# Kernel optimization log

Hardware: AMD Instinct MI355X
Metric: run time of the kernel (lower is better)

## Reference

```python
import jax, jax.numpy as jnp
import numpy as np

H = 5  # hidden size
SEQ = 512
BATCH = 16384


def _lstm_layer(x, Wih, Whh, bih, bhh):
    # x: (B, S, D_in); weights follow PyTorch layout: W (4H, D), gate order i,f,g,o
    B = x.shape[0]
    b = bih + bhh
    xs = jnp.swapaxes(x, 0, 1)  # (S, B, D_in)
    # precompute input projections for all timesteps: (S, B, 4H)
    xproj = jnp.einsum('sbd,gd->sbg', xs, Wih) + b

    def step(carry, xp):
        h, c = carry
        gates = xp + h @ Whh.T  # (B, 4H)
        i, f, g, o = jnp.split(gates, 4, axis=-1)
        i = jax.nn.sigmoid(i)
        f = jax.nn.sigmoid(f)
        g = jnp.tanh(g)
        o = jax.nn.sigmoid(o)
        c = f * c + i * g
        h = o * jnp.tanh(c)
        return (h, c), h

    h0 = jnp.zeros((B, H), dtype=x.dtype)
    c0 = jnp.zeros((B, H), dtype=x.dtype)
    _, hs = jax.lax.scan(step, (h0, c0), xproj)  # hs: (S, B, H)
    return jnp.swapaxes(hs, 0, 1)  # (B, S, H)


def setup_inputs() -> dict:
    key = jax.random.key(0)
    ks = jax.random.split(key, 13)
    s = 1.0 / np.sqrt(H)
    u = lambda k, shp: jax.random.uniform(k, shp, jnp.float32, -s, s)
    return {
        'x': jax.random.normal(ks[0], (BATCH, SEQ, 1), jnp.float32),
        'Wih0': u(ks[1], (4 * H, 1)),
        'Whh0': u(ks[2], (4 * H, H)),
        'bih0': u(ks[3], (4 * H,)),
        'bhh0': u(ks[4], (4 * H,)),
        'Wih1': u(ks[5], (4 * H, H)),
        'Whh1': u(ks[6], (4 * H, H)),
        'bih1': u(ks[7], (4 * H,)),
        'bhh1': u(ks[8], (4 * H,)),
        'W1': jax.random.uniform(ks[9], (512, SEQ * H), jnp.float32, -1 / np.sqrt(SEQ * H), 1 / np.sqrt(SEQ * H)),
        'b1': jax.random.uniform(ks[10], (512,), jnp.float32, -1 / np.sqrt(SEQ * H), 1 / np.sqrt(SEQ * H)),
        'W2': jax.random.uniform(ks[11], (1, 512), jnp.float32, -1 / np.sqrt(512), 1 / np.sqrt(512)),
        'b2': jax.random.uniform(ks[12], (1,), jnp.float32, -1 / np.sqrt(512), 1 / np.sqrt(512)),
    }


def reference(x, Wih0, Whh0, bih0, bhh0, Wih1, Whh1, bih1, bhh1, W1, b1, W2, b2):
    h = _lstm_layer(x, Wih0, Whh0, bih0, bhh0)   # (B, S, 5)
    h = _lstm_layer(h, Wih1, Whh1, bih1, bhh1)   # (B, S, 5)
    h = h.reshape(h.shape[0], -1)                # (B, S*5)
    h = h @ W1.T + b1                            # (B, 512)
    out = h @ W2.T + b2                          # (B, 1)
    return out
```

## Files before the change

kernel.cpp:

```cpp
#include <hip/hip_runtime.h>

#define BATCH 16384
#define SEQ 512

typedef float f4 __attribute__((ext_vector_type(4)));
typedef _Float16 half4 __attribute__((ext_vector_type(4)));
typedef _Float16 half8 __attribute__((ext_vector_type(8)));

#define SIGS (-1.44269504088896f)
#define TNHS (-2.88539008177793f)
#define NTNH (2.88539008177793f)

union HB2 { unsigned int u[2]; half4 h; };
union HB4 { unsigned int u[4]; half8 h; };

__device__ __forceinline__ float bpermf(int addr, float v) {
    return __int_as_float(__builtin_amdgcn_ds_bpermute(addr, __float_as_int(v)));
}
__device__ __forceinline__ unsigned int h16(float v) {
    return (unsigned int)__builtin_bit_cast(unsigned short, (_Float16)v);
}
__device__ __forceinline__ unsigned int pk2(float a, float b) {
    return __builtin_bit_cast(unsigned int, __builtin_amdgcn_cvt_pkrtz(a, b));
}
__device__ __forceinline__ unsigned int lolo(unsigned int a, unsigned int b) {
    return __builtin_amdgcn_perm(b, a, 0x05040100u);
}

__global__ __launch_bounds__(256) void collapse_kernel(
    const float* __restrict__ W1, const float* __restrict__ b1,
    const float* __restrict__ W2, const float* __restrict__ b2,
    float* __restrict__ ws)
{
    const int kl = threadIdx.x & 15;
    const int ms = threadIdx.x >> 4;
    const int k  = blockIdx.x * 16 + kl;
    const float* w1p = W1 + (size_t)(ms * 32) * 2560 + k;
    const float* w2p = W2 + ms * 32;
    float acc = 0.f;
    #pragma unroll 8
    for (int m = 0; m < 32; ++m) acc = fmaf(w2p[m], w1p[(size_t)m * 2560], acc);
    __shared__ float red[16][17];
    red[ms][kl] = acc;
    __syncthreads();
    if (ms == 0) {
        float s = 0.f;
        #pragma unroll
        for (int r = 0; r < 16; ++r) s += red[r][kl];
        const int t = k / 5, u = k % 5;
        if (u < 4) ws[(u << 10) + 2 * t] = s;
        else {
            ws[2*t + 1] = s;        ws[1024 + 2*t + 1] = s;
            ws[2048 + 2*t + 1] = s; ws[3072 + 2*t + 1] = s;
        }
    }
    if (blockIdx.x == 0) {
        const int t = threadIdx.x;
        float p = fmaf(W2[t], b1[t], W2[t + 256] * b1[t + 256]);
        #pragma unroll
        for (int off = 32; off > 0; off >>= 1) p += __shfl_down(p, off);
        __shared__ float cred[4];
        if ((t & 63) == 0) cred[t >> 6] = p;
        __syncthreads();
        if (t == 0) ws[4096] = cred[0] + cred[1] + cred[2] + cred[3] + b2[0];
    }
}

__global__ __launch_bounds__(64)
__attribute__((amdgpu_waves_per_eu(1, 1)))
void lstm_fused_kernel(
    const float* __restrict__ x,
    const float* __restrict__ Wih0, const float* __restrict__ Whh0,
    const float* __restrict__ bih0, const float* __restrict__ bhh0,
    const float* __restrict__ Wih1, const float* __restrict__ Whh1,
    const float* __restrict__ bih1, const float* __restrict__ bhh1,
    const float* __restrict__ ws, float* __restrict__ out)
{
    const int lane = threadIdx.x;
    const int e15  = lane & 15;
    const int g    = lane >> 4;
    const int e    = blockIdx.x * 16 + e15;
    const float sc[4] = {SIGS, SIGS, TNHS, SIGS};

    HB2 aL0a, aL1a;
    HB4 aU;
    {
        const int m = e15;
        {
            const int u = m >> 2, gi = m & 3, gr = gi * 5 + u;
            const float s = sc[gi];
            float w0 = Whh0[gr * 5 + g];
            float w1 = (g == 0) ? Wih0[gr] : (g == 1 ? Whh0[gr * 5 + 4] : 0.f);
            aL0a.u[0] = h16(w0 * s) | (h16(w1 * s) << 16);
            aL0a.u[1] = 0u;
        }
        {
            const int u = m >> 2, gi = m & 3, gr = gi * 5 + u;
            const float s = sc[gi];
            float w0 = Wih1[gr * 5 + g];
            float w1 = Whh1[gr * 5 + g];
            float w2 = (g == 1) ? Wih1[gr * 5 + 4] : (g == 2 ? Whh1[gr * 5 + 4] : 0.f);
            aL1a.u[0] = h16(w0 * s) | (h16(w1 * s) << 16);
            aL1a.u[1] = h16(w2 * s);
        }
        {
            float w0 = 0.f, w1 = 0.f, s = 0.f;
            if (m >= 4 && m < 8) {
                const int gi = m - 4, gr = gi * 5 + 4;
                s = sc[gi];
                w0 = Whh0[gr * 5 + g];
                w1 = (g == 0) ? Wih0[gr] : (g == 1 ? Whh0[gr * 5 + 4] : 0.f);
            }
            aU.u[0] = h16(w0 * s) | (h16(w1 * s) << 16);
            aU.u[1] = 0u;
        }
        {
            float w0 = 0.f, w1 = 0.f, w2 = 0.f, s = 0.f;
            if (m >= 8 && m < 12) {
                const int gi = m - 8, gr = gi * 5 + 4;
                s = sc[gi];
                w0 = Wih1[gr * 5 + g];
                w1 = Whh1[gr * 5 + g];
                w2 = (g == 1) ? Wih1[gr * 5 + 4] : (g == 2 ? Whh1[gr * 5 + 4] : 0.f);
            }
            aU.u[2] = h16(w0 * s) | (h16(w1 * s) << 16);
            aU.u[3] = h16(w2 * s);
        }
    }
    f4 cL0a, cL1a, cbm;
    #pragma unroll
    for (int r = 0; r < 4; ++r) {
        cL0a[r] = (bih0[r*5+g] + bhh0[r*5+g]) * sc[r];
        cL1a[r] = (bih1[r*5+g] + bhh1[r*5+g]) * sc[r];
        cbm[r]  = (g == 1) ? (bih0[r*5+4] + bhh0[r*5+4]) * sc[r]
                : (g == 2) ? (bih1[r*5+4] + bhh1[r*5+4]) * sc[r] : 0.f;
    }

    const float* xp  = x + (size_t)e * SEQ;
    const float* wsg = ws + (g << 10);
    const bool isg0 = (g == 0), isg2 = (g == 2);
    const unsigned selA = isg0 ? 0x05040100u : 0x03020100u;
    const unsigned selB = isg0 ? 0x07060100u : 0x03020100u;

    float cs0 = 0.f, cs1 = 0.f, cs4 = 0.f, acc = 0.f, acc4 = 0.f;
    f4 dA, dC, dU;

    {
        float2 x01 = *(const float2*)xp;
        unsigned xh0 = h16(x01.x), xh1 = h16(x01.y);
        HB2 b0; b0.u[0] = isg0 ? (xh0 << 16) : 0u; b0.u[1] = 0u;
        dA = __builtin_amdgcn_mfma_f32_16x16x16f16(aL0a.h, b0.h, cL0a, 0, 0, 0);
        HB4 bu0; bu0.u[0] = b0.u[0]; bu0.u[1] = bu0.u[2] = bu0.u[3] = 0u;
        dU = __builtin_amdgcn_mfma_f32_16x16x32_f16(aU.h, bu0.h, cbm, 0, 0, 0);
        float A0 = __builtin_amdgcn_exp2f(dA[0]), F0 = __builtin_amdgcn_exp2f(dA[1]);
        float B0 = __builtin_amdgcn_exp2f(dA[2]), O0 = __builtin_amdgcn_exp2f(dA[3]);
        float A1 = __builtin_amdgcn_exp2f(dU[0]), F1 = __builtin_amdgcn_exp2f(dU[1]);
        float B1 = __builtin_amdgcn_exp2f(dU[2]), O1 = __builtin_amdgcn_exp2f(dU[3]);
        float t0 = 1.f + A0, t1 = 1.f + A1;
        float ab0 = fmaf(t0, B0, t0), ab1 = fmaf(t1, B1, t1);
        float D0 = fmaf(ab0, F0, ab0), D1 = fmaf(ab1, F1, ab1);
        float r0 = __builtin_amdgcn_rcpf(D0), r1 = __builtin_amdgcn_rcpf(D1);
        float bs0 = fmaf(B0, NTNH, TNHS), bs1 = fmaf(B1, NTNH, TNHS);
        float w0 = fmaf(bs0, F0, bs0), w1 = fmaf(bs1, F1, bs1);
        cs0 = fmaf(ab0, cs0, w0) * r0;
        cs4 = fmaf(ab1, cs4, w1) * r1;
        float Ce0 = __builtin_amdgcn_exp2f(fminf(cs0, 17.f));
        float Ce1 = __builtin_amdgcn_exp2f(fminf(cs4, 17.f));
        float o0 = 1.f + O0, o1 = 1.f + O1;
        float e0 = fmaf(o0, Ce0, o0), e1 = fmaf(o1, Ce1, o1);
        float hA = (1.f - Ce0) * __builtin_amdgcn_rcpf(e0);
        float h4 = (1.f - Ce1) * __builtin_amdgcn_rcpf(e1);
        if (isg2) { h4 = 0.f; cs4 = 0.f; }
        unsigned hx0 = pk2(hA, h4);
        HB2 B0n, B1n;
        B0n.u[0] = isg0 ? lolo(hx0, xh1) : hx0;  B0n.u[1] = 0u;
        dA = __builtin_amdgcn_mfma_f32_16x16x16f16(aL0a.h, B0n.h, cL0a, 0, 0, 0);
        B1n.u[0] = pk2(hA, 0.f);  B1n.u[1] = hx0 >> 16;
        HB4 BU; BU.u[0] = B0n.u[0]; BU.u[1] = 0u; BU.u[2] = B1n.u[0]; BU.u[3] = B1n.u[1];
        dU = __builtin_amdgcn_mfma_f32_16x16x32_f16(aU.h, BU.h, cbm, 0, 0, 0);
        dC = __builtin_amdgcn_mfma_f32_16x16x16f16(aL1a.h, B1n.h, cL1a, 0, 0, 0);
    }

    auto body = [&](unsigned xpair, unsigned sel, float wMu, float w4u) {
        float A0 = __builtin_amdgcn_exp2f(dA[0]), F0 = __builtin_amdgcn_exp2f(dA[1]);
        float B0 = __builtin_amdgcn_exp2f(dA[2]), O0 = __builtin_amdgcn_exp2f(dA[3]);
        float A1 = __builtin_amdgcn_exp2f(dU[0]), F1 = __builtin_amdgcn_exp2f(dU[1]);
        float B1 = __builtin_amdgcn_exp2f(dU[2]), O1 = __builtin_amdgcn_exp2f(dU[3]);
        float A2 = __builtin_amdgcn_exp2f(dC[0]), F2 = __builtin_amdgcn_exp2f(dC[1]);
        float B2 = __builtin_amdgcn_exp2f(dC[2]), O2 = __builtin_amdgcn_exp2f(dC[3]);
        float t0 = 1.f + A0, t1 = 1.f + A1, t2 = 1.f + A2;
        float ab0 = fmaf(t0, B0, t0), ab1 = fmaf(t1, B1, t1), ab2 = fmaf(t2, B2, t2);
        float D0 = fmaf(ab0, F0, ab0), D1 = fmaf(ab1, F1, ab1), D2 = fmaf(ab2, F2, ab2);
        float r01 = __builtin_amdgcn_rcpf(D0 * D1);
        float r0 = r01 * D1, r1 = r01 * D0;
        float r2 = __builtin_amdgcn_rcpf(D2);
        float bs0 = fmaf(B0, NTNH, TNHS), bs1 = fmaf(B1, NTNH, TNHS), bs2 = fmaf(B2, NTNH, TNHS);
        float w0 = fmaf(bs0, F0, bs0), w1 = fmaf(bs1, F1, bs1), w2 = fmaf(bs2, F2, bs2);
        cs0 = fmaf(ab0, cs0, w0) * r0;
        cs4 = fmaf(ab1, cs4, w1) * r1;
        cs1 = fmaf(ab2, cs1, w2) * r2;
        float Ce2 = __builtin_amdgcn_exp2f(fminf(cs1, 17.f));
        float o2 = 1.f + O2;
        float e2 = fmaf(o2, Ce2, o2);
        float hC = (1.f - Ce2) * __builtin_amdgcn_rcpf(e2);
        acc  = fmaf(hC, wMu, acc);
        float Ce0 = __builtin_amdgcn_exp2f(fminf(cs0, 17.f));
        float Ce1 = __builtin_amdgcn_exp2f(fminf(cs4, 17.f));
        float o0 = 1.f + O0, o1 = 1.f + O1;
        float e0 = fmaf(o0, Ce0, o0), e1 = fmaf(o1, Ce1, o1);
        float rr = __builtin_amdgcn_rcpf(e0 * e1);
        float hA = (1.f - Ce0) * (rr * e1);
        float h4 = (1.f - Ce1) * (rr * e0);
        acc4 = fmaf(h4, w4u, acc4);
        unsigned hx0  = pk2(hA, h4);
        unsigned b1lo = pk2(hA, hC);
        unsigned b1hi = hx0 >> 16;
        HB2 B0n;
        B0n.u[0] = __builtin_amdgcn_perm(xpair, hx0, sel);  B0n.u[1] = 0u;
        dA = __builtin_amdgcn_mfma_f32_16x16x16f16(aL0a.h, B0n.h, cL0a, 0, 0, 0);
        HB4 BU; BU.u[0] = B0n.u[0]; BU.u[1] = 0u; BU.u[2] = b1lo; BU.u[3] = b1hi;
        dU = __builtin_amdgcn_mfma_f32_16x16x32_f16(aU.h, BU.h, cbm, 0, 0, 0);
        HB2 B1n; B1n.u[0] = b1lo; B1n.u[1] = b1hi;
        dC = __builtin_amdgcn_mfma_f32_16x16x16f16(aL1a.h, B1n.h, cL1a, 0, 0, 0);
    };

    unsigned xqa, xqb;  float4 wqa, wqb;
    {
        float2 xi0 = *(const float2*)(xp + 2);
        float2 xi1 = *(const float2*)(xp + 4);
        xqa = pk2(xi0.x, xi0.y);  xqb = pk2(xi1.x, xi1.y);
        wqa = *(const float4*)(wsg);
        wqb = *(const float4*)(wsg + 4);
    }
    for (int m = 1; m < 502; m += 4) {
        float2 xi0 = *(const float2*)(xp + m + 5);
        float2 xi1 = *(const float2*)(xp + m + 7);
        unsigned nxa = pk2(xi0.x, xi0.y), nxb = pk2(xi1.x, xi1.y);
        float4 nwa = *(const float4*)(wsg + 2 * (m + 3));
        float4 nwb = *(const float4*)(wsg + 2 * (m + 3) + 4);
        body(xqa, selA, wqa.x, wqa.y);
        body(xqa, selB, wqa.z, wqa.w);
        body(xqb, selA, wqb.x, wqb.y);
        body(xqb, selB, wqb.z, wqb.w);
        xqa = nxa; xqb = nxb; wqa = nwa; wqb = nwb;
    }
    {
        unsigned nxa = pk2(xp[510], xp[511]);
        unsigned nxb = pk2(xp[511], xp[511]);
        float4 nwa = *(const float4*)(wsg + 2 * 508);
        float4 nwb = *(const float4*)(wsg + 2 * 508 + 4);
        body(xqa, selA, wqa.x, wqa.y);
        body(xqa, selB, wqa.z, wqa.w);
        body(xqb, selA, wqb.x, wqb.y);
        body(xqb, selB, wqb.z, wqb.w);
        xqa = nxa; xqb = nxb; wqa = nwa; wqb = nwb;
    }
    {
        body(xqa, selA, wqa.x, wqa.y);
        body(xqa, selB, wqa.z, wqa.w);
        body(xqb, selA, wqb.x, wqb.y);
        body(xqb, selB, wqb.z, wqb.w);
    }

    float accT = acc + (isg2 ? acc4 : 0.f);
    float t0 = bpermf(e15 << 2, accT);
    float t1 = bpermf((e15 + 16) << 2, accT);
    float t2 = bpermf((e15 + 32) << 2, accT);
    float t3 = bpermf((e15 + 48) << 2, accT);
    if (lane < 16) out[e] = (t0 + t1) + (t2 + t3) + ws[4096];
}

extern "C" void kernel_launch(void* const* d_in, const int* in_sizes, int n_in,
                              void* d_out, int out_size, void* d_ws, size_t ws_size,
                              hipStream_t stream) {
    const float* x    = (const float*)d_in[0];
    const float* Wih0 = (const float*)d_in[1];
    const float* Whh0 = (const float*)d_in[2];
    const float* bih0 = (const float*)d_in[3];
    const float* bhh0 = (const float*)d_in[4];
    const float* Wih1 = (const float*)d_in[5];
    const float* Whh1 = (const float*)d_in[6];
    const float* bih1 = (const float*)d_in[7];
    const float* bhh1 = (const float*)d_in[8];
    const float* W1   = (const float*)d_in[9];
    const float* b1   = (const float*)d_in[10];
    const float* W2   = (const float*)d_in[11];
    const float* b2   = (const float*)d_in[12];
    float* out = (float*)d_out;
    float* ws  = (float*)d_ws;

    collapse_kernel<<<160, 256, 0, stream>>>(W1, b1, W2, b2, ws);
    lstm_fused_kernel<<<BATCH / 16, 64, 0, stream>>>(x, Wih0, Whh0, bih0, bhh0,
                                                     Wih1, Whh1, bih1, bhh1, ws, out);
}
```

Before: 192.4 us.

## Interleave two independent batch groups per wavefront to hide recurrence latency

Each wavefront now processes two groups of 16 sequences (e and e+8192), interleaving their recurrent step bodies so MFMA and transcendental latency of one chain can overlap with the other. Grid size is halved accordingly. This adds register pressure (duplicated state) and leaves half as many wavefronts, which may reduce occupancy-based latency hiding.

```diff
diff --git a/kernel.cpp b/kernel.cpp
--- a/kernel.cpp
+++ b/kernel.cpp
@@ -136,16 +136,19 @@
                 : (g == 2) ? (bih1[r*5+4] + bhh1[r*5+4]) * sc[r] : 0.f;
     }
 
-    const float* xp  = x + (size_t)e * SEQ;
+    const float* xpP = x + (size_t)e * SEQ;
+    const float* xpQ = xpP + (size_t)8192 * SEQ;
     const float* wsg = ws + (g << 10);
     const bool isg0 = (g == 0), isg2 = (g == 2);
     const unsigned selA = isg0 ? 0x05040100u : 0x03020100u;
     const unsigned selB = isg0 ? 0x07060100u : 0x03020100u;
 
-    float cs0 = 0.f, cs1 = 0.f, cs4 = 0.f, acc = 0.f, acc4 = 0.f;
-    f4 dA, dC, dU;
-
-    {
+    float cs0P = 0.f, cs1P = 0.f, cs4P = 0.f, accP = 0.f, acc4P = 0.f;
+    float cs0Q = 0.f, cs1Q = 0.f, cs4Q = 0.f, accQ = 0.f, acc4Q = 0.f;
+    f4 dAP, dCP, dUP, dAQ, dCQ, dUQ;
+
+    auto prologue = [&](const float* xp, f4& dA, f4& dU, f4& dC,
+                        float& cs0, float& cs4) {
         float2 x01 = *(const float2*)xp;
         unsigned xh0 = h16(x01.x), xh1 = h16(x01.y);
         HB2 b0; b0.u[0] = isg0 ? (xh0 << 16) : 0u; b0.u[1] = 0u;
@@ -179,9 +182,13 @@
         HB4 BU; BU.u[0] = B0n.u[0]; BU.u[1] = 0u; BU.u[2] = B1n.u[0]; BU.u[3] = B1n.u[1];
         dU = __builtin_amdgcn_mfma_f32_16x16x32_f16(aU.h, BU.h, cbm, 0, 0, 0);
         dC = __builtin_amdgcn_mfma_f32_16x16x16f16(aL1a.h, B1n.h, cL1a, 0, 0, 0);
-    }
-
-    auto body = [&](unsigned xpair, unsigned sel, float wMu, float w4u) {
+    };
+    prologue(xpP, dAP, dUP, dCP, cs0P, cs4P);
+    prologue(xpQ, dAQ, dUQ, dCQ, cs0Q, cs4Q);
+
+    auto body = [&](f4& dA, f4& dU, f4& dC, float& cs0, float& cs4, float& cs1,
+                    float& acc, float& acc4,
+                    unsigned xpair, unsigned sel, float wMu, float w4u) {
         float A0 = __builtin_amdgcn_exp2f(dA[0]), F0 = __builtin_amdgcn_exp2f(dA[1]);
         float B0 = __builtin_amdgcn_exp2f(dA[2]), O0 = __builtin_amdgcn_exp2f(dA[3]);
         float A1 = __builtin_amdgcn_exp2f(dU[0]), F1 = __builtin_amdgcn_exp2f(dU[1]);
@@ -224,50 +231,68 @@
         dC = __builtin_amdgcn_mfma_f32_16x16x16f16(aL1a.h, B1n.h, cL1a, 0, 0, 0);
     };
 
-    unsigned xqa, xqb;  float4 wqa, wqb;
-    {
-        float2 xi0 = *(const float2*)(xp + 2);
-        float2 xi1 = *(const float2*)(xp + 4);
-        xqa = pk2(xi0.x, xi0.y);  xqb = pk2(xi1.x, xi1.y);
+    #define BODY_P(xq, sl, wm, w4) body(dAP, dUP, dCP, cs0P, cs4P, cs1P, accP, acc4P, xq, sl, wm, w4)
+    #define BODY_Q(xq, sl, wm, w4) body(dAQ, dUQ, dCQ, cs0Q, cs4Q, cs1Q, accQ, acc4Q, xq, sl, wm, w4)
+
+    unsigned xqaP, xqbP, xqaQ, xqbQ;  float4 wqa, wqb;
+    {
+        float2 pa = *(const float2*)(xpP + 2), pb = *(const float2*)(xpP + 4);
+        float2 qa = *(const float2*)(xpQ + 2), qb = *(const float2*)(xpQ + 4);
+        xqaP = pk2(pa.x, pa.y);  xqbP = pk2(pb.x, pb.y);
+        xqaQ = pk2(qa.x, qa.y);  xqbQ = pk2(qb.x, qb.y);
         wqa = *(const float4*)(wsg);
         wqb = *(const float4*)(wsg + 4);
     }
     for (int m = 1; m < 502; m += 4) {
-        float2 xi0 = *(const float2*)(xp + m + 5);
-        float2 xi1 = *(const float2*)(xp + m + 7);
-        unsigned nxa = pk2(xi0.x, xi0.y), nxb = pk2(xi1.x, xi1.y);
+        float2 pa = *(const float2*)(xpP + m + 5), pb = *(const float2*)(xpP + m + 7);
+        float2 qa = *(const float2*)(xpQ + m + 5), qb = *(const float2*)(xpQ + m + 7);
+        unsigned nxaP = pk2(pa.x, pa.y), nxbP = pk2(pb.x, pb.y);
+        unsigned nxaQ = pk2(qa.x, qa.y), nxbQ = pk2(qb.x, qb.y);
         float4 nwa = *(const float4*)(wsg + 2 * (m + 3));
         float4 nwb = *(const float4*)(wsg + 2 * (m + 3) + 4);
-        body(xqa, selA, wqa.x, wqa.y);
-        body(xqa, selB, wqa.z, wqa.w);
-        body(xqb, selA, wqb.x, wqb.y);
-        body(xqb, selB, wqb.z, wqb.w);
-        xqa = nxa; xqb = nxb; wqa = nwa; wqb = nwb;
-    }
-    {
-        unsigned nxa = pk2(xp[510], xp[511]);
-        unsigned nxb = pk2(xp[511], xp[511]);
+        BODY_P(xqaP, selA, wqa.x, wqa.y);  BODY_Q(xqaQ, selA, wqa.x, wqa.y);
+        BODY_P(xqaP, selB, wqa.z, wqa.w);  BODY_Q(xqaQ, selB, wqa.z, wqa.w);
+        BODY_P(xqbP, selA, wqb.x, wqb.y);  BODY_Q(xqbQ, selA, wqb.x, wqb.y);
+        BODY_P(xqbP, selB, wqb.z, wqb.w);  BODY_Q(xqbQ, selB, wqb.z, wqb.w);
+        xqaP = nxaP; xqbP = nxbP; xqaQ = nxaQ; xqbQ = nxbQ; wqa = nwa; wqb = nwb;
+    }
+    {
+        unsigned nxaP = pk2(xpP[510], xpP[511]), nxbP = pk2(xpP[511], xpP[511]);
+        unsigned nxaQ = pk2(xpQ[510], xpQ[511]), nxbQ = pk2(xpQ[511], xpQ[511]);
         float4 nwa = *(const float4*)(wsg + 2 * 508);
         float4 nwb = *(const float4*)(wsg + 2 * 508 + 4);
-        body(xqa, selA, wqa.x, wqa.y);
-        body(xqa, selB, wqa.z, wqa.w);
-        body(xqb, selA, wqb.x, wqb.y);
-        body(xqb, selB, wqb.z, wqb.w);
-        xqa = nxa; xqb = nxb; wqa = nwa; wqb = nwb;
-    }
-    {
-        body(xqa, selA, wqa.x, wqa.y);
-        body(xqa, selB, wqa.z, wqa.w);
-        body(xqb, selA, wqb.x, wqb.y);
-        body(xqb, selB, wqb.z, wqb.w);
-    }
-
-    float accT = acc + (isg2 ? acc4 : 0.f);
-    float t0 = bpermf(e15 << 2, accT);
-    float t1 = bpermf((e15 + 16) << 2, accT);
-    float t2 = bpermf((e15 + 32) << 2, accT);
-    float t3 = bpermf((e15 + 48) << 2, accT);
-    if (lane < 16) out[e] = (t0 + t1) + (t2 + t3) + ws[4096];
+        BODY_P(xqaP, selA, wqa.x, wqa.y);  BODY_Q(xqaQ, selA, wqa.x, wqa.y);
+        BODY_P(xqaP, selB, wqa.z, wqa.w);  BODY_Q(xqaQ, selB, wqa.z, wqa.w);
+        BODY_P(xqbP, selA, wqb.x, wqb.y);  BODY_Q(xqbQ, selA, wqb.x, wqb.y);
+        BODY_P(xqbP, selB, wqb.z, wqb.w);  BODY_Q(xqbQ, selB, wqb.z, wqb.w);
+        xqaP = nxaP; xqbP = nxbP; xqaQ = nxaQ; xqbQ = nxbQ; wqa = nwa; wqb = nwb;
+    }
+    {
+        BODY_P(xqaP, selA, wqa.x, wqa.y);  BODY_Q(xqaQ, selA, wqa.x, wqa.y);
+        BODY_P(xqaP, selB, wqa.z, wqa.w);  BODY_Q(xqaQ, selB, wqa.z, wqa.w);
+        BODY_P(xqbP, selA, wqb.x, wqb.y);  BODY_Q(xqbQ, selA, wqb.x, wqb.y);
+        BODY_P(xqbP, selB, wqb.z, wqb.w);  BODY_Q(xqbQ, selB, wqb.z, wqb.w);
+    }
+    #undef BODY_P
+    #undef BODY_Q
+
+    const float cbias = ws[4096];
+    {
+        float accT = accP + (isg2 ? acc4P : 0.f);
+        float t0 = bpermf(e15 << 2, accT);
+        float t1 = bpermf((e15 + 16) << 2, accT);
+        float t2 = bpermf((e15 + 32) << 2, accT);
+        float t3 = bpermf((e15 + 48) << 2, accT);
+        if (lane < 16) out[e] = (t0 + t1) + (t2 + t3) + cbias;
+    }
+    {
+        float accT = accQ + (isg2 ? acc4Q : 0.f);
+        float t0 = bpermf(e15 << 2, accT);
+        float t1 = bpermf((e15 + 16) << 2, accT);
+        float t2 = bpermf((e15 + 32) << 2, accT);
+        float t3 = bpermf((e15 + 48) << 2, accT);
+        if (lane < 16) out[e + 8192] = (t0 + t1) + (t2 + t3) + cbias;
+    }
 }
 
 extern "C" void kernel_launch(void* const* d_in, const int* in_sizes, int n_in,
@@ -290,6 +315,6 @@
     float* ws  = (float*)d_ws;
 
     collapse_kernel<<<160, 256, 0, stream>>>(W1, b1, W2, b2, ws);
-    lstm_fused_kernel<<<BATCH / 16, 64, 0, stream>>>(x, Wih0, Whh0, bih0, bhh0,
+    lstm_fused_kernel<<<BATCH / 32, 64, 0, stream>>>(x, Wih0, Whh0, bih0, bhh0,
                                                      Wih1, Whh1, bih1, bhh1, ws, out);
 }
```

Measured after the change: 269.7 us. 40.2% more time.
